# Optimization experiments

Measured on AMD Instinct MI355X. Metric: run time of the kernel, lower is better.

Reference implementation:

```python
import jax, jax.numpy as jnp
import numpy as np

B, IN, N_NEURONS, DEG = 16384, 256, 64, 7  # batch, input_dim, output_dim (neurons), max_degree
D = IN * (DEG + 1)  # cumulative Chebyshev basis width per sample


def setup_inputs() -> dict:
    key = jax.random.key(0)
    k1, k2, _ = jax.random.split(key, 3)
    x = jax.random.normal(k1, (B, IN), dtype=jnp.float32)
    # per-neuron least-squares coefficients [(deg+1)*input_dim] -> stored as [N, D]
    coeffs = jax.random.normal(k2, (N_NEURONS, D), dtype=jnp.float32) * 0.05
    # horizontal_weight per neuron (nn.Parameter initialized to ones(1))
    hweights = jnp.ones((N_NEURONS,), dtype=jnp.float32)
    return {"x": x, "coeffs": coeffs, "hweights": hweights}


def _cheb_basis(t, deg):
    """Chebyshev T_0..T_deg via recurrence. t: [B, IN] in [-1,1] -> [B, IN, deg+1]."""
    polys = [jnp.ones_like(t), t]
    for _ in range(2, deg + 1):
        polys.append(2.0 * t * polys[-1] - polys[-2])
    return jnp.stack(polys[: deg + 1], axis=-1)


def reference(x, coeffs, hweights):
    # KANNeuron.forward: tanh squash, then cumulative Chebyshev transform
    t = jnp.tanh(x)  # [B, IN]
    # torch code builds, per input dim, stack of T_0..T_deg then cats over dims:
    # layout is dim-major -> reshape of [B, IN, DEG+1] matches exactly
    T = _cheb_basis(t, DEG).reshape(x.shape[0], D)  # [B, D]
    # per-neuron: hweight_n * (T @ c_n); layer: stack over neurons, sum(dim=0)
    Y = T @ (coeffs * hweights[:, None]).T  # [B, N]
    return Y.sum(axis=1, keepdims=True)  # [B, 1] (source sums stacked neuron outputs)
```

## Files before the change

### kernel.cpp

```cpp
#include <hip/hip_runtime.h>


constexpr int B_SAMPLES = 16384;
constexpr int IN_DIM    = 256;
constexpr int N_NEURONS = 64;
constexpr int DEGP1     = 8;
constexpr int D_FEAT    = IN_DIM * DEGP1;

__global__ __launch_bounds__(256) void kan_reduce_w(const float* __restrict__ coeffs,
                                                    const float* __restrict__ hw,
                                                    float* __restrict__ w) {
    int d = blockIdx.x * 256 + threadIdx.x;
    if (d >= D_FEAT) return;
    float acc = 0.f;
#pragma unroll
    for (int n = 0; n < N_NEURONS; ++n)
        acc = fmaf(coeffs[n * D_FEAT + d], hw[n], acc);
    w[d] = acc;
}

constexpr int SPB = 16;

__global__ __launch_bounds__(256) void kan_fwd(const float* __restrict__ x,
                                               const float* __restrict__ w,
                                               float* __restrict__ out) {
    const int tid  = threadIdx.x;
    const int lane = tid & 63;
    const int wave = tid >> 6;
    const int b0   = blockIdx.x * SPB;

    const float4 wlo = *reinterpret_cast<const float4*>(w + tid * DEGP1);
    const float4 whi = *reinterpret_cast<const float4*>(w + tid * DEGP1 + 4);

    __shared__ float red[SPB][4];

    for (int s = 0; s < SPB; ++s) {
        const int b = b0 + s;
        const float t = tanhf(x[(size_t)b * IN_DIM + tid]);

        const float t2 = 2.f * t;
        float Tm2 = 1.f, Tm1 = t;
        float acc = fmaf(wlo.y, t, wlo.x);
        float T;
        T = t2 * Tm1 - Tm2; acc = fmaf(wlo.z, T, acc); Tm2 = Tm1; Tm1 = T;
        T = t2 * Tm1 - Tm2; acc = fmaf(wlo.w, T, acc); Tm2 = Tm1; Tm1 = T;
        T = t2 * Tm1 - Tm2; acc = fmaf(whi.x, T, acc); Tm2 = Tm1; Tm1 = T;
        T = t2 * Tm1 - Tm2; acc = fmaf(whi.y, T, acc); Tm2 = Tm1; Tm1 = T;
        T = t2 * Tm1 - Tm2; acc = fmaf(whi.z, T, acc); Tm2 = Tm1; Tm1 = T;
        T = t2 * Tm1 - Tm2; acc = fmaf(whi.w, T, acc);

#pragma unroll
        for (int off = 32; off > 0; off >>= 1)
            acc += __shfl_down(acc, off, 64);
        if (lane == 0) red[s][wave] = acc;
    }
    __syncthreads();
    if (tid < SPB) {
        out[b0 + tid] = red[tid][0] + red[tid][1] + red[tid][2] + red[tid][3];
    }
}

extern "C" void kernel_launch(void* const* d_in, const int* in_sizes, int n_in,
                              void* d_out, int out_size, void* d_ws, size_t ws_size,
                              hipStream_t stream) {
    const float* x      = (const float*)d_in[0];
    const float* coeffs = (const float*)d_in[1];
    const float* hw     = (const float*)d_in[2];
    float* out = (float*)d_out;
    float* w   = (float*)d_ws;

    kan_reduce_w<<<(D_FEAT + 255) / 256, 256, 0, stream>>>(coeffs, hw, w);
    kan_fwd<<<B_SAMPLES / SPB, 256, 0, stream>>>(x, w, out);
}
```

Before: 20.53 us.

## Assign whole samples to waves, vectorize x loads, use fast tanh

The forward kernel now gives each wave a full sample: every lane loads four consecutive x values as a float4 and holds the matching 32 reduced weights in registers. The shared-memory reduction and block barrier are replaced by one wave shuffle reduction and a direct store. tanhf is swapped for an exp and reciprocal approximation, and the weight-reduction kernel switches to float4 loads. This cuts the per-sample barrier and reduction work and the cost of the transcendental, at the price of higher register pressure and slightly lower tanh accuracy.

```diff
diff --git a/kernel.cpp b/kernel.cpp
--- a/kernel.cpp
+++ b/kernel.cpp
@@ -7,16 +7,28 @@
 constexpr int DEGP1     = 8;
 constexpr int D_FEAT    = IN_DIM * DEGP1;
 
+__device__ __forceinline__ float fast_tanh(float v) {
+    float e = __expf(2.0f * v);
+    return 1.0f - 2.0f * __builtin_amdgcn_rcpf(e + 1.0f);
+}
+
 __global__ __launch_bounds__(256) void kan_reduce_w(const float* __restrict__ coeffs,
                                                     const float* __restrict__ hw,
                                                     float* __restrict__ w) {
-    int d = blockIdx.x * 256 + threadIdx.x;
-    if (d >= D_FEAT) return;
-    float acc = 0.f;
+    int d4 = blockIdx.x * 256 + threadIdx.x;
+    if (d4 >= D_FEAT / 4) return;
+    const float4* c4 = reinterpret_cast<const float4*>(coeffs);
+    float4 acc = {0.f, 0.f, 0.f, 0.f};
 #pragma unroll
-    for (int n = 0; n < N_NEURONS; ++n)
-        acc = fmaf(coeffs[n * D_FEAT + d], hw[n], acc);
-    w[d] = acc;
+    for (int n = 0; n < N_NEURONS; ++n) {
+        float h = hw[n];
+        float4 c = c4[n * (D_FEAT / 4) + d4];
+        acc.x = fmaf(c.x, h, acc.x);
+        acc.y = fmaf(c.y, h, acc.y);
+        acc.z = fmaf(c.z, h, acc.z);
+        acc.w = fmaf(c.w, h, acc.w);
+    }
+    reinterpret_cast<float4*>(w)[d4] = acc;
 }
 
 constexpr int SPB = 16;
@@ -26,37 +38,39 @@
                                                float* __restrict__ out) {
     const int tid  = threadIdx.x;
     const int lane = tid & 63;
-    const int wave = tid >> 6;
+    const int wv   = tid >> 6;
     const int b0   = blockIdx.x * SPB;
 
-    const float4 wlo = *reinterpret_cast<const float4*>(w + tid * DEGP1);
-    const float4 whi = *reinterpret_cast<const float4*>(w + tid * DEGP1 + 4);
+    const float4* w4 = reinterpret_cast<const float4*>(w) + (size_t)lane * 8;
+    float4 W[4][2];
+#pragma unroll
+    for (int j = 0; j < 4; ++j) { W[j][0] = w4[j * 2]; W[j][1] = w4[j * 2 + 1]; }
 
-    __shared__ float red[SPB][4];
-
-    for (int s = 0; s < SPB; ++s) {
+#pragma unroll
+    for (int s = wv; s < SPB; s += 4) {
         const int b = b0 + s;
-        const float t = tanhf(x[(size_t)b * IN_DIM + tid]);
-
-        const float t2 = 2.f * t;
-        float Tm2 = 1.f, Tm1 = t;
-        float acc = fmaf(wlo.y, t, wlo.x);
-        float T;
-        T = t2 * Tm1 - Tm2; acc = fmaf(wlo.z, T, acc); Tm2 = Tm1; Tm1 = T;
-        T = t2 * Tm1 - Tm2; acc = fmaf(wlo.w, T, acc); Tm2 = Tm1; Tm1 = T;
-        T = t2 * Tm1 - Tm2; acc = fmaf(whi.x, T, acc); Tm2 = Tm1; Tm1 = T;
-        T = t2 * Tm1 - Tm2; acc = fmaf(whi.y, T, acc); Tm2 = Tm1; Tm1 = T;
-        T = t2 * Tm1 - Tm2; acc = fmaf(whi.z, T, acc); Tm2 = Tm1; Tm1 = T;
-        T = t2 * Tm1 - Tm2; acc = fmaf(whi.w, T, acc);
-
+        float4 xv = reinterpret_cast<const float4*>(x + (size_t)b * IN_DIM)[lane];
+        float xs[4] = {xv.x, xv.y, xv.z, xv.w};
+        float acc = 0.f;
+#pragma unroll
+        for (int j = 0; j < 4; ++j) {
+            const float t  = fast_tanh(xs[j]);
+            const float t2 = 2.f * t;
+            const float4 wlo = W[j][0], whi = W[j][1];
+            float Tm2 = 1.f, Tm1 = t, T;
+            float a = fmaf(wlo.y, t, wlo.x);
+            T = t2 * Tm1 - Tm2; a = fmaf(wlo.z, T, a); Tm2 = Tm1; Tm1 = T;
+            T = t2 * Tm1 - Tm2; a = fmaf(wlo.w, T, a); Tm2 = Tm1; Tm1 = T;
+            T = t2 * Tm1 - Tm2; a = fmaf(whi.x, T, a); Tm2 = Tm1; Tm1 = T;
+            T = t2 * Tm1 - Tm2; a = fmaf(whi.y, T, a); Tm2 = Tm1; Tm1 = T;
+            T = t2 * Tm1 - Tm2; a = fmaf(whi.z, T, a); Tm2 = Tm1; Tm1 = T;
+            T = t2 * Tm1 - Tm2; a = fmaf(whi.w, T, a);
+            acc += a;
+        }
 #pragma unroll
         for (int off = 32; off > 0; off >>= 1)
             acc += __shfl_down(acc, off, 64);
-        if (lane == 0) red[s][wave] = acc;
-    }
-    __syncthreads();
-    if (tid < SPB) {
-        out[b0 + tid] = red[tid][0] + red[tid][1] + red[tid][2] + red[tid][3];
+        if (lane == 0) out[b] = acc;
     }
 }
 
@@ -69,6 +83,6 @@
     float* out = (float*)d_out;
     float* w   = (float*)d_ws;
 
-    kan_reduce_w<<<(D_FEAT + 255) / 256, 256, 0, stream>>>(coeffs, hw, w);
+    kan_reduce_w<<<(D_FEAT / 4 + 255) / 256, 256, 0, stream>>>(coeffs, hw, w);
     kan_fwd<<<B_SAMPLES / SPB, 256, 0, stream>>>(x, w, out);
 }
```

Measured after the change: 17.29 us. -15.8%, faster.
